# Performance work log

Hardware: AMD Instinct MI355X
Metric: run time of the kernel (lower is better)

The kernel has to match this reference:

```python
import jax, jax.numpy as jnp
import numpy as np
import itertools
from functools import partial

H, W = 224, 448            # output raster size
R = 2                      # splat_radius
RADIUS_SCALE = 1.5
B, T, V, GH, GW = 1, 2, 2, 56, 112   # batch, time, views, gaussian grid
N = V * GH * GW            # gaussians per (b,t)
OFFSETS = jnp.array(list(itertools.product(range(-R, R + 1), repeat=2)), dtype=jnp.int32)  # (K,2)


def setup_inputs() -> dict:
    key = jax.random.key(0)
    ks = jax.random.split(key, 8)
    center = jax.random.normal(ks[0], (B, T, V, GH, GW, 3), jnp.float32) * 2.0
    scale = jax.random.uniform(ks[1], (B, T, V, GH, GW, 3), jnp.float32) * 0.1
    feat_dc = jax.random.uniform(ks[2], (B, T, V, GH, GW, 3), jnp.float32)
    opacity = jax.random.uniform(ks[3], (B, T, V, GH, GW, 1), jnp.float32)
    background_prob = jax.random.uniform(ks[4], (B, T, V, GH, GW), jnp.float32)
    sem_proj_2d = jax.random.uniform(ks[5], (B, T, V, 3, H, W), jnp.float32)
    # realistic pinhole intrinsics: fx=fy=220, principal point at image center
    camera_intrinsics = jnp.broadcast_to(jnp.array([220.0, 220.0, W / 2.0, H / 2.0], jnp.float32), (B, V, 4))
    # cameras ~5m behind the (origin-centered) point cloud, identity rotation + jittered translation
    trans = jnp.array([0.0, 0.0, -5.0], jnp.float32) + 0.2 * jax.random.normal(ks[6], (B, T, V, 3), jnp.float32)
    c2w = jnp.broadcast_to(jnp.eye(4, dtype=jnp.float32), (B, T, V, 4, 4))
    camera_to_world = c2w.at[..., :3, 3].set(trans)
    first_ego_pose_world = jnp.broadcast_to(jnp.eye(4, dtype=jnp.float32), (B, 4, 4))
    return {"center": center, "scale": scale, "feat_dc": feat_dc, "opacity": opacity,
            "background_prob": background_prob, "sem_proj_2d": sem_proj_2d,
            "camera_intrinsics": camera_intrinsics, "camera_to_world": camera_to_world,
            "first_ego_pose_world": first_ego_pose_world}


def _render_view(world, scale, color, alpha, intr, c2w):
    # world: (N,4) homogeneous world coords; scale,alpha: (N,); color: (N,3)
    fx, fy, cx, cy = intr[0], intr[1], intr[2], intr[3]
    w2c = jnp.linalg.inv(c2w)
    cam = (world @ w2c.T)[:, :3]              # (N,3) camera-frame coords
    z = cam[:, 2]
    finite = jnp.all(jnp.isfinite(cam), axis=-1)
    valid = (z > 1e-3) & finite & (alpha > 1e-5)
    z_safe = jnp.where(valid, z, 1.0)
    u = cam[:, 0] * fx / z_safe + cx
    v = cam[:, 1] * fy / z_safe + cy
    sigma = jnp.clip((fx + fy) * 0.5 * jnp.abs(scale) / jnp.maximum(z_safe, 1e-3), 0.75, 10.0)
    inb = (u >= -R - 1.0) & (u <= W + R) & (v >= -R - 1.0) & (v <= H + R)
    keep = valid & inb
    cnt = jnp.sum(keep)
    sigma_mean = jnp.where(cnt > 0, jnp.sum(jnp.where(keep, sigma, 0.0)) / jnp.maximum(cnt, 1), 0.0)
    a_eff = jnp.where(keep, alpha, 0.0)
    # depth sort front-to-back; dropped points carry zero alpha so their position is irrelevant
    order = jnp.argsort(jnp.where(keep, z, jnp.inf))
    u_s = jnp.where(keep, u, -1e6)[order]
    v_s = jnp.where(keep, v, -1e6)[order]
    sig_s = sigma[order]
    col_s = color[order]
    a_s = a_eff[order]
    x0 = jnp.floor(u_s).astype(jnp.int32)
    y0 = jnp.floor(v_s).astype(jnp.int32)
    radii = jnp.clip(jnp.ceil(sig_s * RADIUS_SCALE), 1, R).astype(jnp.int32)

    def step(carry, pt):
        alpha_den, rgb_num = carry
        x0p, y0p, up, vp, sp, ap, rp, colp = pt
        xo = x0p + OFFSETS[:, 0]
        yo = y0p + OFFSETS[:, 1]
        keep_off = ((jnp.abs(OFFSETS[:, 0]) <= rp) & (jnp.abs(OFFSETS[:, 1]) <= rp)
                    & (xo >= 0) & (xo < W) & (yo >= 0) & (yo < H))
        sp_c = jnp.maximum(sp, 1e-3)
        du = (up - xo.astype(up.dtype)) / sp_c
        dv = (vp - yo.astype(vp.dtype)) / sp_c
        la = jnp.clip(jnp.exp(-0.5 * (du * du + dv * dv)) * ap, 0.0, 0.999)
        idx = jnp.where(keep_off, yo * W + xo, H * W)   # OOB sentinel -> dropped by scatter
        old = alpha_den[jnp.clip(idx, 0, H * W - 1)]
        transmit = jnp.clip(1.0 - old, 0.0, 1.0)
        contrib = jnp.where(keep_off, la * transmit, 0.0)
        alpha_den = alpha_den.at[idx].set(jnp.clip(old + contrib, 0.0, 0.999), mode='drop')
        rgb_num = rgb_num.at[:, idx].add(colp[:, None] * contrib[None, :], mode='drop')
        return (alpha_den, rgb_num), None

    init = (jnp.zeros(H * W, jnp.float32), jnp.zeros((3, H * W), jnp.float32))
    (alpha_den, rgb_num), _ = jax.lax.scan(step, init, (x0, y0, u_s, v_s, sig_s, a_s, radii, col_s))
    touch = jnp.mean((alpha_den > 1e-6).astype(jnp.float32))
    rgb = jnp.clip(rgb_num, 0.0, 1.0).reshape(3, H, W)
    aout = jnp.clip(alpha_den, 0.0, 1.0).reshape(H, W)
    return rgb, aout, sigma_mean, touch


def _render_branch(centers, scales, colors, alpha, intr, c2w, first_pose):
    cf = centers.reshape(B, T, N, 3)
    sf = jnp.mean(scales, axis=-1).reshape(B, T, N)
    colf = jnp.clip(colors.reshape(B, T, N, 3), 0.0, 1.0)
    af = jnp.clip(alpha.reshape(B, T, N), 0.0, 1.0)
    xyz_h = jnp.concatenate([cf, jnp.ones((B, T, N, 1), cf.dtype)], axis=-1)
    world = jnp.einsum('bij,btnj->btni', first_pose, xyz_h)      # (B,T,N,4)
    M = B * T * V
    wv = jnp.broadcast_to(world[:, :, None], (B, T, V, N, 4)).reshape(M, N, 4)
    sv = jnp.broadcast_to(sf[:, :, None], (B, T, V, N)).reshape(M, N)
    cv = jnp.broadcast_to(colf[:, :, None], (B, T, V, N, 3)).reshape(M, N, 3)
    av = jnp.broadcast_to(af[:, :, None], (B, T, V, N)).reshape(M, N)
    iv = jnp.broadcast_to(intr[:, None], (B, T, V, 4)).reshape(M, 4)
    mv = c2w.reshape(M, 4, 4)
    rgb, aout, sm, tr = jax.vmap(_render_view)(wv, sv, cv, av, iv, mv)
    return (rgb.reshape(B, T, V, 3, H, W), aout.reshape(B, T, V, 1, H, W), jnp.mean(sm), jnp.mean(tr))


def reference(center, scale, feat_dc, opacity, background_prob, sem_proj_2d,
              camera_intrinsics, camera_to_world, first_ego_pose_world):
    base_alpha = jnp.clip(opacity[..., 0], 0.0, 1.0)                      # (B,T,V,GH,GW)
    dyn = jnp.clip(1.0 - background_prob.reshape(B, T, V, GH, GW), 0.0, 1.0)
    a_all = base_alpha
    a_dyn = base_alpha * dyn
    a_sta = base_alpha * (1.0 - dyn)
    rgb_all, al_all, sigma_mean, touch = _render_branch(center, scale, feat_dc, a_all, camera_intrinsics, camera_to_world, first_ego_pose_world)
    rgb_dyn, al_dyn, _, _ = _render_branch(center, scale, feat_dc, a_dyn, camera_intrinsics, camera_to_world, first_ego_pose_world)
    rgb_sta, al_sta, _, _ = _render_branch(center, scale, feat_dc, a_sta, camera_intrinsics, camera_to_world, first_ego_pose_world)
    return (rgb_sta, rgb_dyn, rgb_all, al_sta, al_dyn, al_all, sem_proj_2d, sigma_mean, touch)
```

## Files before the change

kernel.cpp:

```cpp
#include <hip/hip_runtime.h>
#include <cmath>

namespace {
constexpr int Hh = 224, Ww = 448;
constexpr int Tt = 2, Vv = 2, GH = 56, GW = 112;
constexpr int Nn = Vv * GH * GW;
constexpr int TV = Tt * Vv;
constexpr int TOT = TV * Nn;
constexpr int HW = Hh * Ww;
constexpr int TILE = 8;
constexpr int NTX = Ww / TILE;
constexpr int NTY = Hh / TILE;
constexpr int NTILES = TV * NTX * NTY;
constexpr int CAP_T = 256;
constexpr int NWAVE_PRE = TOT / 64;
constexpr int WPV = Nn / 64;
constexpr int NCLS = 64;
constexpr int TILES_PER_CLS = NTILES / NCLS;

constexpr size_t RGB_SZ = (size_t)TV * 3 * HW;
constexpr size_t AL_SZ  = (size_t)TV * HW;
constexpr size_t OFF_RGB_STA = 0;
constexpr size_t OFF_RGB_DYN = RGB_SZ;
constexpr size_t OFF_RGB_ALL = 2 * RGB_SZ;
constexpr size_t OFF_AL_STA  = 3 * RGB_SZ;
constexpr size_t OFF_AL_DYN  = 3 * RGB_SZ + AL_SZ;
constexpr size_t OFF_AL_ALL  = 3 * RGB_SZ + 2 * AL_SZ;
constexpr size_t OFF_SEM     = 3 * RGB_SZ + 3 * AL_SZ;
constexpr size_t OFF_SM      = OFF_SEM + RGB_SZ;
constexpr size_t OFF_TOUCH   = OFF_SM + 1;

constexpr size_t WS_FRAG  = 0;
constexpr size_t WS_PSUM  = (size_t)TOT * 12;
constexpr size_t WS_PCNT  = WS_PSUM + NWAVE_PRE;
constexpr size_t WS_CTRS  = WS_PCNT + NWAVE_PRE;
constexpr size_t WS_SLOT  = WS_CTRS;
constexpr size_t WS_CDONE = WS_CTRS + 64 * 16;
constexpr size_t WS_DONE  = WS_CDONE + 64 * 16;
constexpr size_t WS_TCNT  = WS_DONE + 4;
constexpr size_t WS_LIST  = WS_TCNT + NTILES;
constexpr size_t N_CTR_BYTES = (WS_LIST - WS_CTRS) * 4;
}

__device__ inline unsigned long long shfl_xor_u64(unsigned long long x, int m) {
  unsigned int lo = (unsigned int)x, hi = (unsigned int)(x >> 32);
  lo = __shfl_xor(lo, m, 64);
  hi = __shfl_xor(hi, m, 64);
  return ((unsigned long long)hi << 32) | lo;
}

__global__ __launch_bounds__(256) void preprocess_k(
    const float* __restrict__ center, const float* __restrict__ scale,
    const float* __restrict__ feat, const float* __restrict__ opac,
    const float* __restrict__ bg, const float* __restrict__ sem,
    const float* __restrict__ intr, const float* __restrict__ c2w,
    const float* __restrict__ fpose, float* __restrict__ ws,
    float* __restrict__ out) {
#pragma clang fp contract(off)
  const int idx = blockIdx.x * 256 + threadIdx.x;
  const int n  = idx % Nn;
  const int tv = idx / Nn;
  const int v  = tv % Vv;
  const int t  = tv / Vv;
  const size_t gi = (size_t)t * Nn + n;

  float* Wfrag = ws + WS_FRAG;
  float* Wpsum = ws + WS_PSUM;
  int*   Wpcnt = (int*)(ws + WS_PCNT);
  int*   Wtcnt = (int*)(ws + WS_TCNT);
  int*   Wlist = (int*)(ws + WS_LIST);

  {
    const float4* s4 = (const float4*)sem;
    float4* d4 = (float4*)(out + OFF_SEM);
    for (int i = idx; i < (int)(RGB_SZ / 4); i += TOT) d4[i] = s4[i];
  }

  double m00, m01, m02, m03, m10, m11, m12, m13,
         m20, m21, m22, m23, m30, m31, m32, m33;
  {
    const float* C = c2w + (size_t)tv * 16;
    m00 = C[0];  m01 = C[1];  m02 = C[2];  m03 = C[3];
    m10 = C[4];  m11 = C[5];  m12 = C[6];  m13 = C[7];
    m20 = C[8];  m21 = C[9];  m22 = C[10]; m23 = C[11];
    m30 = C[12]; m31 = C[13]; m32 = C[14]; m33 = C[15];
  }
  const double s0d = m00 * m11 - m10 * m01;
  const double s1d = m00 * m12 - m10 * m02;
  const double s2d = m00 * m13 - m10 * m03;
  const double s3d = m01 * m12 - m11 * m02;
  const double s4d = m01 * m13 - m11 * m03;
  const double s5d = m02 * m13 - m12 * m03;
  const double c5d = m22 * m33 - m32 * m23;
  const double c4d = m21 * m33 - m31 * m23;
  const double c3d = m21 * m32 - m31 * m22;
  const double c2d = m20 * m33 - m30 * m23;
  const double c1d = m20 * m32 - m30 * m22;
  const double c0d = m20 * m31 - m30 * m21;
  const double invdet =
      1.0 / (s0d * c5d - s1d * c4d + s2d * c3d + s3d * c2d - s4d * c1d + s5d * c0d);
  const float M0  = (float)(( m11 * c5d - m12 * c4d + m13 * c3d) * invdet);
  const float M1  = (float)((-m01 * c5d + m02 * c4d - m03 * c3d) * invdet);
  const float M2  = (float)(( m31 * s5d - m32 * s4d + m33 * s3d) * invdet);
  const float M3  = (float)((-m21 * s5d + m22 * s4d - m23 * s3d) * invdet);
  const float M4  = (float)((-m10 * c5d + m12 * c2d - m13 * c1d) * invdet);
  const float M5  = (float)(( m00 * c5d - m02 * c2d + m03 * c1d) * invdet);
  const float M6  = (float)((-m30 * s5d + m32 * s2d - m33 * s1d) * invdet);
  const float M7  = (float)(( m20 * s5d - m22 * s2d + m23 * s1d) * invdet);
  const float M8  = (float)(( m10 * c4d - m11 * c2d + m13 * c0d) * invdet);
  const float M9  = (float)((-m00 * c4d + m01 * c2d - m03 * c0d) * invdet);
  const float M10 = (float)(( m30 * s4d - m31 * s2d + m33 * s0d) * invdet);
  const float M11 = (float)((-m20 * s4d + m21 * s2d - m23 * s0d) * invdet);

  const float c0 = center[gi * 3 + 0], c1 = center[gi * 3 + 1], c2 = center[gi * 3 + 2];
  const float s0 = scale[gi * 3 + 0], s1 = scale[gi * 3 + 1], s2 = scale[gi * 3 + 2];
  const float sf = ((s0 + s1) + s2) / 3.0f;
  const float colr = fminf(fmaxf(feat[gi * 3 + 0], 0.0f), 1.0f);
  const float colg = fminf(fmaxf(feat[gi * 3 + 1], 0.0f), 1.0f);
  const float colb = fminf(fmaxf(feat[gi * 3 + 2], 0.0f), 1.0f);
  const float base = fminf(fmaxf(opac[gi], 0.0f), 1.0f);
  const float dyn  = fminf(fmaxf(1.0f - bg[gi], 0.0f), 1.0f);
  const float aAll = base;
  const float aDyn = base * dyn;
  const float aSta = base * (1.0f - dyn);

  const float wd0 = ((fpose[0]  * c0 + fpose[1]  * c1) + fpose[2]  * c2) + fpose[3];
  const float wd1 = ((fpose[4]  * c0 + fpose[5]  * c1) + fpose[6]  * c2) + fpose[7];
  const float wd2 = ((fpose[8]  * c0 + fpose[9]  * c1) + fpose[10] * c2) + fpose[11];
  const float wd3 = ((fpose[12] * c0 + fpose[13] * c1) + fpose[14] * c2) + fpose[15];

  const float cam0 = ((M0 * wd0 + M1 * wd1) + M2  * wd2) + M3  * wd3;
  const float cam1 = ((M4 * wd0 + M5 * wd1) + M6  * wd2) + M7  * wd3;
  const float cam2 = ((M8 * wd0 + M9 * wd1) + M10 * wd2) + M11 * wd3;
  const bool fin = (fabsf(cam0) <= 3.4028235e38f) && (fabsf(cam1) <= 3.4028235e38f) &&
                   (fabsf(cam2) <= 3.4028235e38f);
  const float z = cam2;
  const float fx = intr[v * 4 + 0], fy = intr[v * 4 + 1];
  const float ppx = intr[v * 4 + 2], ppy = intr[v * 4 + 3];

  bool kept = false;
  float u = 0.0f, vv2 = 0.0f, sig = 0.0f;
  if ((z > 0.001f) && fin) {
    u   = cam0 * fx / z + ppx;
    vv2 = cam1 * fy / z + ppy;
    float tsc = (fx + fy) * 0.5f;
    sig = tsc * fabsf(sf);
    sig = sig / fmaxf(z, 0.001f);
    sig = fminf(fmaxf(sig, 0.75f), 10.0f);
    const bool inb = (u >= -3.0f) && (u <= 450.0f) && (vv2 >= -3.0f) && (vv2 <= 226.0f);
    kept = inb && (aAll > 1e-5f);
  }

  if (kept) {
    const int x0 = (int)floorf(u);
    const int y0 = (int)floorf(vv2);
    const float rc = ceilf(sig * 1.5f);
    const int rad = rc < 1.0f ? 1 : (rc > 2.0f ? 2 : (int)rc);
    const int pk = ((x0 + 4) << 16) | ((y0 + 4) << 4) | rad;
    float4* F = (float4*)Wfrag + (size_t)idx * 3;
    F[0] = make_float4(u, vv2, 1.0f / sig, z);
    F[1] = make_float4(colr, colg, colb, __int_as_float(pk));
    F[2] = make_float4(aAll, aDyn, aSta, 0.0f);
    const int x_lo = x0 - rad, x_hi = x0 + rad;
    const int y_lo = y0 - rad, y_hi = y0 + rad;
    if (x_hi >= 0 && x_lo < Ww && y_hi >= 0 && y_lo < Hh) {
      const int tx_lo = (x_lo > 0 ? x_lo : 0) >> 3;
      const int tx_hi = (x_hi < Ww - 1 ? x_hi : Ww - 1) >> 3;
      const int ty_lo = (y_lo > 0 ? y_lo : 0) >> 3;
      const int ty_hi = (y_hi < Hh - 1 ? y_hi : Hh - 1) >> 3;
      for (int ty = ty_lo; ty <= ty_hi; ++ty)
        for (int tx = tx_lo; tx <= tx_hi; ++tx) {
          const int tile = (tv * NTY + ty) * NTX + tx;
          const int slot = atomicAdd(&Wtcnt[tile], 1);
          if (slot < CAP_T) Wlist[(size_t)tile * CAP_T + slot] = n;
        }
    }
  }

  float sred = kept ? sig : 0.0f;
  int   cred = kept ? 1 : 0;
  #pragma unroll
  for (int off = 32; off > 0; off >>= 1) {
    sred += __shfl_down(sred, off, 64);
    cred += __shfl_down(cred, off, 64);
  }
  if ((threadIdx.x & 63) == 0) {
    const int w = idx >> 6;
    Wpsum[w] = sred; Wpcnt[w] = cred;
  }
}

__global__ __launch_bounds__(64) void raster_k(float* __restrict__ ws,
                                               float* __restrict__ out) {
#pragma clang fp contract(off)
  __shared__ unsigned long long s_key[CAP_T];
  __shared__ float4 s_f0[64], s_f1[64], s_f2[64];

  const int tid = threadIdx.x;
  const int tv  = blockIdx.z;
  const int px  = blockIdx.x * TILE + (tid & 7);
  const int py  = blockIdx.y * TILE + (tid >> 3);
  const float fpx = (float)px, fpy = (float)py;
  const size_t base = (size_t)tv * Nn;

  const float* Wfrag = ws + WS_FRAG;
  const float* Wpsum = ws + WS_PSUM;
  const int*   Wpcnt = (const int*)(ws + WS_PCNT);
  int*   Wslot  = (int*)(ws + WS_SLOT);
  int*   Wcdone = (int*)(ws + WS_CDONE);
  int*   Wdone  = (int*)(ws + WS_DONE);
  const int* Wtcnt = (const int*)(ws + WS_TCNT);
  const int* Wlist = (const int*)(ws + WS_LIST);

  const int tile = (tv * NTY + blockIdx.y) * NTX + blockIdx.x;
  const int cnt0 = Wtcnt[tile];
  const int cnt  = cnt0 < CAP_T ? cnt0 : CAP_T;
  const int* mylist = Wlist + (size_t)tile * CAP_T;

  float Aall = 0.0f, Adyn = 0.0f, Asta = 0.0f;
  float Ra = 0.0f, Ga = 0.0f, Ba = 0.0f;
  float Rd = 0.0f, Gd = 0.0f, Bd = 0.0f;
  float Rs = 0.0f, Gs = 0.0f, Bs = 0.0f;

  auto composite = [&](int m) {
    for (int j = 0; j < m; ++j) {
      const float4 f1 = s_f1[j];
      const int pk  = __float_as_int(f1.w);
      const int rad = pk & 15;
      const int y0  = ((pk >> 4) & 0xfff) - 4;
      const int x0  = (pk >> 16) - 4;
      if (abs(px - x0) <= rad && abs(py - y0) <= rad) {
        const float4 f0 = s_f0[j];
        const float du = (f0.x - fpx) * f0.z;
        const float dv = (f0.y - fpy) * f0.z;
        const float gs = __expf(-0.5f * (du * du + dv * dv));
        const float4 f2 = s_f2[j];
        {
          const float la = fminf(fmaxf(gs * f2.x, 0.0f), 0.999f);
          const float tr = fminf(fmaxf(1.0f - Aall, 0.0f), 1.0f);
          const float ct = la * tr;
          Ra += f1.x * ct; Ga += f1.y * ct; Ba += f1.z * ct;
          Aall = fminf(fmaxf(Aall + ct, 0.0f), 0.999f);
        }
        if (f2.y > 1e-5f) {
          const float la = fminf(fmaxf(gs * f2.y, 0.0f), 0.999f);
          const float tr = fminf(fmaxf(1.0f - Adyn, 0.0f), 1.0f);
          const float ct = la * tr;
          Rd += f1.x * ct; Gd += f1.y * ct; Bd += f1.z * ct;
          Adyn = fminf(fmaxf(Adyn + ct, 0.0f), 0.999f);
        }
        if (f2.z > 1e-5f) {
          const float la = fminf(fmaxf(gs * f2.z, 0.0f), 0.999f);
          const float tr = fminf(fmaxf(1.0f - Asta, 0.0f), 1.0f);
          const float ct = la * tr;
          Rs += f1.x * ct; Gs += f1.y * ct; Bs += f1.z * ct;
          Asta = fminf(fmaxf(Asta + ct, 0.0f), 0.999f);
        }
      }
    }
  };

  if (cnt <= 64) {
    unsigned long long key = ~0ULL;
    if (tid < cnt) {
      const unsigned int n = (unsigned int)mylist[tid];
      key = ((unsigned long long)__float_as_uint(Wfrag[(base + n) * 12 + 3]) << 32) | n;
    }
    if (cnt > 1) {
      int P = 1;
      while (P < cnt) P <<= 1;
      for (int k = 2; k <= P; k <<= 1) {
        for (int j = k >> 1; j > 0; j >>= 1) {
          const unsigned long long other = shfl_xor_u64(key, j);
          const bool up = ((tid & k) == 0);
          const bool keep_min = (up == ((tid & j) == 0));
          key = keep_min ? (key < other ? key : other) : (key > other ? key : other);
        }
      }
    }
    if (tid < cnt) {
      const int n = (int)(key & 0xffffffffULL);
      const float4* F = (const float4*)Wfrag + (size_t)(base + n) * 3;
      s_f0[tid] = F[0]; s_f1[tid] = F[1]; s_f2[tid] = F[2];
    }
    __syncthreads();
    composite(cnt);
  } else {
    for (int i = tid; i < cnt; i += 64) {
      const unsigned int n = (unsigned int)mylist[i];
      s_key[i] = ((unsigned long long)__float_as_uint(Wfrag[(base + n) * 12 + 3]) << 32) | n;
    }
    int P = 1;
    while (P < cnt) P <<= 1;
    for (int i = cnt + tid; i < P; i += 64) s_key[i] = ~0ULL;
    __syncthreads();
    for (int k = 2; k <= P; k <<= 1) {
      for (int j = k >> 1; j > 0; j >>= 1) {
        for (int i = tid; i < P; i += 64) {
          const int ixj = i ^ j;
          if (ixj > i) {
            const unsigned long long a = s_key[i], b2 = s_key[ixj];
            const bool up = ((i & k) == 0);
            if ((a > b2) == up) { s_key[i] = b2; s_key[ixj] = a; }
          }
        }
        __syncthreads();
      }
    }
    for (int cb = 0; cb < cnt; cb += 64) {
      const int m = min(64, cnt - cb);
      if (tid < m) {
        const int n = (int)(s_key[cb + tid] & 0xffffffffULL);
        const float4* F = (const float4*)Wfrag + (size_t)(base + n) * 3;
        s_f0[tid] = F[0]; s_f1[tid] = F[1]; s_f2[tid] = F[2];
      }
      __syncthreads();
      composite(m);
      __syncthreads();
    }
  }

  const size_t pix = (size_t)py * Ww + px;
  const size_t hw  = (size_t)HW;
  const size_t m3  = (size_t)tv * 3;
  out[OFF_RGB_STA + (m3 + 0) * hw + pix] = fminf(fmaxf(Rs, 0.0f), 1.0f);
  out[OFF_RGB_STA + (m3 + 1) * hw + pix] = fminf(fmaxf(Gs, 0.0f), 1.0f);
  out[OFF_RGB_STA + (m3 + 2) * hw + pix] = fminf(fmaxf(Bs, 0.0f), 1.0f);
  out[OFF_RGB_DYN + (m3 + 0) * hw + pix] = fminf(fmaxf(Rd, 0.0f), 1.0f);
  out[OFF_RGB_DYN + (m3 + 1) * hw + pix] = fminf(fmaxf(Gd, 0.0f), 1.0f);
  out[OFF_RGB_DYN + (m3 + 2) * hw + pix] = fminf(fmaxf(Bd, 0.0f), 1.0f);
  out[OFF_RGB_ALL + (m3 + 0) * hw + pix] = fminf(fmaxf(Ra, 0.0f), 1.0f);
  out[OFF_RGB_ALL + (m3 + 1) * hw + pix] = fminf(fmaxf(Ga, 0.0f), 1.0f);
  out[OFF_RGB_ALL + (m3 + 2) * hw + pix] = fminf(fmaxf(Ba, 0.0f), 1.0f);
  out[OFF_AL_STA + (size_t)tv * hw + pix] = fminf(fmaxf(Asta, 0.0f), 1.0f);
  out[OFF_AL_DYN + (size_t)tv * hw + pix] = fminf(fmaxf(Adyn, 0.0f), 1.0f);
  out[OFF_AL_ALL + (size_t)tv * hw + pix] = fminf(fmaxf(Aall, 0.0f), 1.0f);

  const unsigned long long bal = __ballot(Aall > 1e-6f);
  if (tid == 0) {
    const int my  = (int)__popcll(bal);
    const int cls = tile & (NCLS - 1);
    const int tld = atomicAdd(&Wslot[cls * 16], my);
    asm volatile("s_waitcnt vmcnt(0)" : : "v"(tld) : "memory");
    const int cd = atomicAdd(&Wcdone[cls * 16], 1);
    if (cd == TILES_PER_CLS - 1) {
      asm volatile("s_waitcnt vmcnt(0)" : : "v"(cd) : "memory");
      const int d = atomicAdd(Wdone, 1);
      if (d == NCLS - 1) {
        int acc = 0;
        for (int i = 0; i < NCLS; ++i) acc += atomicAdd(&Wslot[i * 16], 0);
        float sm = 0.0f;
        for (int tvv = 0; tvv < TV; ++tvv) {
          float ps = 0.0f; int pc = 0;
          for (int w = tvv * WPV; w < (tvv + 1) * WPV; ++w) {
            ps += Wpsum[w]; pc += Wpcnt[w];
          }
          sm += (pc > 0) ? (ps / (float)(pc > 1 ? pc : 1)) : 0.0f;
        }
        out[OFF_SM]    = sm / (float)TV;
        out[OFF_TOUCH] = (float)acc / (float)(HW * TV);
      }
    }
  }
}

extern "C" void kernel_launch(void* const* d_in, const int* in_sizes, int n_in,
                              void* d_out, int out_size, void* d_ws, size_t ws_size,
                              hipStream_t stream) {
  const float* center = (const float*)d_in[0];
  const float* scale  = (const float*)d_in[1];
  const float* feat   = (const float*)d_in[2];
  const float* opac   = (const float*)d_in[3];
  const float* bg     = (const float*)d_in[4];
  const float* sem    = (const float*)d_in[5];
  const float* intr   = (const float*)d_in[6];
  const float* c2w    = (const float*)d_in[7];
  const float* fpose  = (const float*)d_in[8];
  float* out = (float*)d_out;
  float* ws  = (float*)d_ws;

  hipMemsetAsync((void*)(ws + WS_CTRS), 0, N_CTR_BYTES, stream);
  hipLaunchKernelGGL(preprocess_k, dim3(TOT / 256), dim3(256), 0, stream,
                     center, scale, feat, opac, bg, sem, intr, c2w, fpose, ws, out);
  hipLaunchKernelGGL(raster_k, dim3(NTX, NTY, TV), dim3(64), 0, stream, ws, out);
}
```

Baseline: 137.5 us.

## Pack four raster tiles per 256-thread block with per-wave LDS and fences

The raster kernel now launches 256-thread blocks in which each of the four waves handles its own 8x8 tile, each with a private slice of LDS. Block-wide barriers inside the sort and compositing are replaced by wave-local lgkmcnt waits. The touch-count reduction is combined across the four waves before a single atomic per block, and the completion classes are regrouped to match the new block count. This cuts the block count and the global atomics by a factor of four. The trade-off is that waves in a block can finish at different times, and it relies on wave-local LDS ordering being correct without a barrier.

After: 139.9 us. No clear change (+1.8%).

```diff
diff --git a/kernel.cpp b/kernel.cpp
--- a/kernel.cpp
+++ b/kernel.cpp
@@ -12,11 +12,14 @@
 constexpr int NTX = Ww / TILE;
 constexpr int NTY = Hh / TILE;
 constexpr int NTILES = TV * NTX * NTY;
+constexpr int NBX = NTX / 2;
+constexpr int NBY = NTY / 2;
+constexpr int NBLK_R = NBX * NBY * TV;
 constexpr int CAP_T = 256;
 constexpr int NWAVE_PRE = TOT / 64;
 constexpr int WPV = Nn / 64;
-constexpr int NCLS = 64;
-constexpr int TILES_PER_CLS = NTILES / NCLS;
+constexpr int NCLS = 56;
+constexpr int BLK_PER_CLS = NBLK_R / NCLS;
 
 constexpr size_t RGB_SZ = (size_t)TV * 3 * HW;
 constexpr size_t AL_SZ  = (size_t)TV * HW;
@@ -35,8 +38,8 @@
 constexpr size_t WS_PCNT  = WS_PSUM + NWAVE_PRE;
 constexpr size_t WS_CTRS  = WS_PCNT + NWAVE_PRE;
 constexpr size_t WS_SLOT  = WS_CTRS;
-constexpr size_t WS_CDONE = WS_CTRS + 64 * 16;
-constexpr size_t WS_DONE  = WS_CDONE + 64 * 16;
+constexpr size_t WS_CDONE = WS_CTRS + NCLS * 16;
+constexpr size_t WS_DONE  = WS_CDONE + NCLS * 16;
 constexpr size_t WS_TCNT  = WS_DONE + 4;
 constexpr size_t WS_LIST  = WS_TCNT + NTILES;
 constexpr size_t N_CTR_BYTES = (WS_LIST - WS_CTRS) * 4;
@@ -47,6 +50,10 @@
   lo = __shfl_xor(lo, m, 64);
   hi = __shfl_xor(hi, m, 64);
   return ((unsigned long long)hi << 32) | lo;
+}
+
+__device__ inline void wave_lds_fence() {
+  asm volatile("s_waitcnt lgkmcnt(0)" ::: "memory");
 }
 
 __global__ __launch_bounds__(256) void preprocess_k(
@@ -190,16 +197,21 @@
   }
 }
 
-__global__ __launch_bounds__(64) void raster_k(float* __restrict__ ws,
-                                               float* __restrict__ out) {
+__global__ __launch_bounds__(256) void raster_k(float* __restrict__ ws,
+                                                float* __restrict__ out) {
 #pragma clang fp contract(off)
-  __shared__ unsigned long long s_key[CAP_T];
-  __shared__ float4 s_f0[64], s_f1[64], s_f2[64];
-
-  const int tid = threadIdx.x;
-  const int tv  = blockIdx.z;
-  const int px  = blockIdx.x * TILE + (tid & 7);
-  const int py  = blockIdx.y * TILE + (tid >> 3);
+  __shared__ unsigned long long s_key[4][CAP_T];
+  __shared__ float4 s_f0[4][64], s_f1[4][64], s_f2[4][64];
+  __shared__ int s_tch[4];
+
+  const int tid  = threadIdx.x;
+  const int w    = tid >> 6;
+  const int lane = tid & 63;
+  const int tv   = blockIdx.z;
+  const int tx   = blockIdx.x * 2 + (w & 1);
+  const int ty   = blockIdx.y * 2 + (w >> 1);
+  const int px   = tx * TILE + (lane & 7);
+  const int py   = ty * TILE + (lane >> 3);
   const float fpx = (float)px, fpy = (float)py;
   const size_t base = (size_t)tv * Nn;
 
@@ -212,7 +224,7 @@
   const int* Wtcnt = (const int*)(ws + WS_TCNT);
   const int* Wlist = (const int*)(ws + WS_LIST);
 
-  const int tile = (tv * NTY + blockIdx.y) * NTX + blockIdx.x;
+  const int tile = (tv * NTY + ty) * NTX + tx;
   const int cnt0 = Wtcnt[tile];
   const int cnt  = cnt0 < CAP_T ? cnt0 : CAP_T;
   const int* mylist = Wlist + (size_t)tile * CAP_T;
@@ -224,17 +236,17 @@
 
   auto composite = [&](int m) {
     for (int j = 0; j < m; ++j) {
-      const float4 f1 = s_f1[j];
+      const float4 f1 = s_f1[w][j];
       const int pk  = __float_as_int(f1.w);
       const int rad = pk & 15;
       const int y0  = ((pk >> 4) & 0xfff) - 4;
       const int x0  = (pk >> 16) - 4;
       if (abs(px - x0) <= rad && abs(py - y0) <= rad) {
-        const float4 f0 = s_f0[j];
+        const float4 f0 = s_f0[w][j];
         const float du = (f0.x - fpx) * f0.z;
         const float dv = (f0.y - fpy) * f0.z;
         const float gs = __expf(-0.5f * (du * du + dv * dv));
-        const float4 f2 = s_f2[j];
+        const float4 f2 = s_f2[w][j];
         {
           const float la = fminf(fmaxf(gs * f2.x, 0.0f), 0.999f);
           const float tr = fminf(fmaxf(1.0f - Aall, 0.0f), 1.0f);
@@ -262,8 +274,8 @@
 
   if (cnt <= 64) {
     unsigned long long key = ~0ULL;
-    if (tid < cnt) {
-      const unsigned int n = (unsigned int)mylist[tid];
+    if (lane < cnt) {
+      const unsigned int n = (unsigned int)mylist[lane];
       key = ((unsigned long long)__float_as_uint(Wfrag[(base + n) * 12 + 3]) << 32) | n;
     }
     if (cnt > 1) {
@@ -272,51 +284,51 @@
       for (int k = 2; k <= P; k <<= 1) {
         for (int j = k >> 1; j > 0; j >>= 1) {
           const unsigned long long other = shfl_xor_u64(key, j);
-          const bool up = ((tid & k) == 0);
-          const bool keep_min = (up == ((tid & j) == 0));
+          const bool up = ((lane & k) == 0);
+          const bool keep_min = (up == ((lane & j) == 0));
           key = keep_min ? (key < other ? key : other) : (key > other ? key : other);
         }
       }
     }
-    if (tid < cnt) {
+    if (lane < cnt) {
       const int n = (int)(key & 0xffffffffULL);
       const float4* F = (const float4*)Wfrag + (size_t)(base + n) * 3;
-      s_f0[tid] = F[0]; s_f1[tid] = F[1]; s_f2[tid] = F[2];
-    }
-    __syncthreads();
+      s_f0[w][lane] = F[0]; s_f1[w][lane] = F[1]; s_f2[w][lane] = F[2];
+    }
+    wave_lds_fence();
     composite(cnt);
   } else {
-    for (int i = tid; i < cnt; i += 64) {
+    for (int i = lane; i < cnt; i += 64) {
       const unsigned int n = (unsigned int)mylist[i];
-      s_key[i] = ((unsigned long long)__float_as_uint(Wfrag[(base + n) * 12 + 3]) << 32) | n;
+      s_key[w][i] = ((unsigned long long)__float_as_uint(Wfrag[(base + n) * 12 + 3]) << 32) | n;
     }
     int P = 1;
     while (P < cnt) P <<= 1;
-    for (int i = cnt + tid; i < P; i += 64) s_key[i] = ~0ULL;
-    __syncthreads();
+    for (int i = cnt + lane; i < P; i += 64) s_key[w][i] = ~0ULL;
+    wave_lds_fence();
     for (int k = 2; k <= P; k <<= 1) {
       for (int j = k >> 1; j > 0; j >>= 1) {
-        for (int i = tid; i < P; i += 64) {
+        for (int i = lane; i < P; i += 64) {
           const int ixj = i ^ j;
           if (ixj > i) {
-            const unsigned long long a = s_key[i], b2 = s_key[ixj];
+            const unsigned long long a = s_key[w][i], b2 = s_key[w][ixj];
             const bool up = ((i & k) == 0);
-            if ((a > b2) == up) { s_key[i] = b2; s_key[ixj] = a; }
+            if ((a > b2) == up) { s_key[w][i] = b2; s_key[w][ixj] = a; }
           }
         }
-        __syncthreads();
+        wave_lds_fence();
       }
     }
     for (int cb = 0; cb < cnt; cb += 64) {
       const int m = min(64, cnt - cb);
-      if (tid < m) {
-        const int n = (int)(s_key[cb + tid] & 0xffffffffULL);
+      if (lane < m) {
+        const int n = (int)(s_key[w][cb + lane] & 0xffffffffULL);
         const float4* F = (const float4*)Wfrag + (size_t)(base + n) * 3;
-        s_f0[tid] = F[0]; s_f1[tid] = F[1]; s_f2[tid] = F[2];
+        s_f0[w][lane] = F[0]; s_f1[w][lane] = F[1]; s_f2[w][lane] = F[2];
       }
-      __syncthreads();
+      wave_lds_fence();
       composite(m);
-      __syncthreads();
+      wave_lds_fence();
     }
   }
 
@@ -337,13 +349,16 @@
   out[OFF_AL_ALL + (size_t)tv * hw + pix] = fminf(fmaxf(Aall, 0.0f), 1.0f);
 
   const unsigned long long bal = __ballot(Aall > 1e-6f);
+  if (lane == 0) s_tch[w] = (int)__popcll(bal);
+  __syncthreads();
   if (tid == 0) {
-    const int my  = (int)__popcll(bal);
-    const int cls = tile & (NCLS - 1);
+    const int my = s_tch[0] + s_tch[1] + s_tch[2] + s_tch[3];
+    const int b  = (blockIdx.z * NBY + blockIdx.y) * NBX + blockIdx.x;
+    const int cls = b % NCLS;
     const int tld = atomicAdd(&Wslot[cls * 16], my);
     asm volatile("s_waitcnt vmcnt(0)" : : "v"(tld) : "memory");
     const int cd = atomicAdd(&Wcdone[cls * 16], 1);
-    if (cd == TILES_PER_CLS - 1) {
+    if (cd == BLK_PER_CLS - 1) {
       asm volatile("s_waitcnt vmcnt(0)" : : "v"(cd) : "memory");
       const int d = atomicAdd(Wdone, 1);
       if (d == NCLS - 1) {
@@ -352,8 +367,8 @@
         float sm = 0.0f;
         for (int tvv = 0; tvv < TV; ++tvv) {
           float ps = 0.0f; int pc = 0;
-          for (int w = tvv * WPV; w < (tvv + 1) * WPV; ++w) {
-            ps += Wpsum[w]; pc += Wpcnt[w];
+          for (int wv2 = tvv * WPV; wv2 < (tvv + 1) * WPV; ++wv2) {
+            ps += Wpsum[wv2]; pc += Wpcnt[wv2];
           }
           sm += (pc > 0) ? (ps / (float)(pc > 1 ? pc : 1)) : 0.0f;
         }
@@ -382,5 +397,5 @@
   hipMemsetAsync((void*)(ws + WS_CTRS), 0, N_CTR_BYTES, stream);
   hipLaunchKernelGGL(preprocess_k, dim3(TOT / 256), dim3(256), 0, stream,
                      center, scale, feat, opac, bg, sem, intr, c2w, fpose, ws, out);
-  hipLaunchKernelGGL(raster_k, dim3(NTX, NTY, TV), dim3(64), 0, stream, ws, out);
-}
+  hipLaunchKernelGGL(raster_k, dim3(NBX, NBY, TV), dim3(256), 0, stream, ws, out);
+}
```
